# Optimization experiments

Hardware: AMD Instinct MI355X
Metric: run time of the kernel (lower is better)

The kernel has to match this reference:

```python
import jax, jax.numpy as jnp
import numpy as np

N, E, B, L = 65536, 262144, 512, 1000
IN_DIM, HID, VOCAB = 74, 128, 25
CHANNELS = [HID, 96, 128, IN_DIM, HID]  # protein conv1d filter chain


def _conv1d(x, k):
    # x: [B, C_in, L], k: [C_out, C_in, 3], stride 1, padding 1 (like nn.Conv1d)
    return jax.lax.conv_general_dilated(x, k, (1,), ((1, 1),),
                                        dimension_numbers=('NCH', 'OIH', 'NCH'))


def setup_inputs() -> dict:
    key = jax.random.key(0)
    ks = jax.random.split(key, 20)

    def gl(k, shape, fan_in):
        return jax.random.normal(k, shape, jnp.float32) / np.float32(np.sqrt(fan_in))

    inp = {}
    inp['node_feats'] = jax.random.normal(ks[0], (N, IN_DIM), jnp.float32)
    # GraphConv (conv1): weight [in, hid]
    inp['W_gc'] = gl(ks[1], (IN_DIM, HID), IN_DIM)
    inp['b_gc'] = jnp.zeros((HID,), jnp.float32)
    # MLPNodeReadout: two linears (no activation between, per dgllife default)
    inp['W_ro_in'] = gl(ks[2], (HID, HID), HID)
    inp['b_ro_in'] = jnp.zeros((HID,), jnp.float32)
    inp['W_ro_out'] = gl(ks[3], (HID, HID), HID)
    inp['b_ro_out'] = jnp.zeros((HID,), jnp.float32)
    inp['Wc1'] = gl(ks[4], (HID, HID), HID); inp['bc1'] = jnp.zeros((HID,), jnp.float32)
    inp['Wc2'] = gl(ks[5], (HID, HID), HID); inp['bc2'] = jnp.zeros((HID,), jnp.float32)
    # protein embedding + 4 conv1d layers
    inp['embed'] = jax.random.normal(ks[6], (VOCAB, HID), jnp.float32)
    for i in range(4):
        cin, cout = CHANNELS[i], CHANNELS[i + 1]
        inp['K%d' % (i + 1)] = gl(ks[7 + i], (cout, cin, 3), cin * 3)
        inp['cb%d' % (i + 1)] = jnp.zeros((cout,), jnp.float32)
    # CPI head: Linear(2h,2h)+ReLU, Linear(2h,1)+Sigmoid
    inp['Wf1'] = gl(ks[11], (2 * HID, 2 * HID), 2 * HID); inp['bf1'] = jnp.zeros((2 * HID,), jnp.float32)
    inp['Wf2'] = gl(ks[12], (2 * HID, 1), 2 * HID); inp['bf2'] = jnp.zeros((1,), jnp.float32)
    # graph structure / protein tokens
    inp['edge_src'] = jax.random.randint(ks[13], (E,), 0, N, jnp.int32)
    inp['edge_dst'] = jax.random.randint(ks[14], (E,), 0, N, jnp.int32)
    inp['graph_ids'] = jnp.sort(jax.random.randint(ks[15], (N,), 0, B, jnp.int32))
    inp['protein_seq'] = jax.random.randint(ks[16], (B, L), 0, VOCAB, jnp.int32)
    return inp


def reference(node_feats, W_gc, b_gc, W_ro_in, b_ro_in, W_ro_out, b_ro_out,
              Wc1, bc1, Wc2, bc2, embed, K1, cb1, K2, cb2, K3, cb3, K4, cb4,
              Wf1, bf1, Wf2, bf2, edge_src, edge_dst, graph_ids, protein_seq):
    n = node_feats.shape[0]
    nb = protein_seq.shape[0]
    # dgl.add_self_loop: append self edges
    loop = jnp.arange(n, dtype=edge_src.dtype)
    src = jnp.concatenate([edge_src, loop])
    dst = jnp.concatenate([edge_dst, loop])
    ones = jnp.ones(src.shape[0], jnp.float32)
    deg_out = jax.ops.segment_sum(ones, src, n)  # out-degree (src norm)
    deg_in = jax.ops.segment_sum(ones, dst, n)   # in-degree (dst norm)
    h = node_feats * jax.lax.rsqrt(deg_out)[:, None]
    h = jax.ops.segment_sum(h[src], dst, n) * jax.lax.rsqrt(deg_in)[:, None]
    h = jax.nn.relu(h @ W_gc + b_gc)
    # MLPNodeReadout (sum over nodes per graph), then outer ReLU
    x = (h @ W_ro_in + b_ro_in) @ W_ro_out + b_ro_out
    hg = jax.nn.relu(jax.ops.segment_sum(x, graph_ids, nb))  # [B, HID]
    # compound FC layers (dropout = identity)
    cv = jax.nn.relu(hg @ Wc1 + bc1)
    cv = jax.nn.relu(cv @ Wc2 + bc2)
    pv = jnp.transpose(embed[protein_seq], (0, 2, 1))
    for K, b in ((K1, cb1), (K2, cb2), (K3, cb3), (K4, cb4)):
        pv = jax.nn.relu(_conv1d(pv, K) + b[None, :, None])
    pmax = jnp.max(pv, axis=-1)  # adaptive_max_pool1d(output_size=1) + squeeze
    # CPI head
    z = jnp.concatenate([cv, pmax], axis=1)  # [B, 2*HID]
    z = jax.nn.relu(z @ Wf1 + bf1)
    return jax.nn.sigmoid(z @ Wf2 + bf2)  # [B, 1]
```

## Files before the change

### kernel.cpp

```cpp
#include <hip/hip_runtime.h>
#include <math.h>

#define IN_DIM 74
#define HID 128
#define LSEQ 1000
#define RSA 272
#define RSB 208
#define TILE 50
#define R0 58
#define R1 56
#define R2 54
#define R3 52
#define NCHUNK 42
#define NGRP 14
#define WBUF_SZ 24576
#define LDS_BIAS 49152
#define LDS_ACT  50944
#define ACTA_SZ  15776
#define ACTB_SZ  11648
#define ACTB_BASE (LDS_ACT + 4*ACTA_SZ)
#define LDS_TOTAL (ACTB_BASE + 4*ACTB_SZ)

typedef unsigned int u32;
typedef unsigned short u16;

typedef __attribute__((ext_vector_type(8))) short bf16x8;
typedef __attribute__((ext_vector_type(4))) float f32x4;

__device__ __forceinline__ u16 f2bf(float f){
  u32 u = __float_as_uint(f);
  u32 r = (u + 0x7fffu + ((u >> 16) & 1u)) >> 16;
  return (u16)r;
}
__device__ __forceinline__ u32 pack2(float x, float y){
  return (u32)f2bf(x) | ((u32)f2bf(y) << 16);
}

__global__ void k_cnt_edge(const int* __restrict__ src, const int* __restrict__ dst,
                           int* out_cnt, int* in_cnt, int E){
  int e = blockIdx.x*256 + threadIdx.x;
  if (e < E){ atomicAdd(&out_cnt[src[e]], 1); atomicAdd(&in_cnt[dst[e]], 1); }
}
__global__ void k_nfs(const float* __restrict__ nf, const int* __restrict__ out_cnt,
                      float* __restrict__ nfs, int total){
  int idx = blockIdx.x*256 + threadIdx.x;
  if (idx < total){
    int i = idx / IN_DIM;
    nfs[idx] = nf[idx] * rsqrtf((float)out_cnt[i] + 1.f);
  }
}
__global__ void k_scan1(const int* __restrict__ cnt, int* pref, int* bsum, int N){
  __shared__ int buf[256];
  int t = threadIdx.x, i = blockIdx.x*256 + t;
  int v = (i < N) ? cnt[i] : 0;
  buf[t] = v; __syncthreads();
  for (int o = 1; o < 256; o <<= 1){
    int tv = (t >= o) ? buf[t-o] : 0;
    __syncthreads(); buf[t] += tv; __syncthreads();
  }
  if (i < N) pref[i] = buf[t] - v;
  if (t == 255) bsum[blockIdx.x] = buf[255];
}
__global__ void k_scan2(int* bsum, int nb){
  __shared__ int buf[1024];
  int t = threadIdx.x;
  int v = (t < nb) ? bsum[t] : 0;
  buf[t] = v; __syncthreads();
  for (int o = 1; o < 1024; o <<= 1){
    int tv = (t >= o) ? buf[t-o] : 0;
    __syncthreads(); buf[t] += tv; __syncthreads();
  }
  if (t < nb) bsum[t] = buf[t] - v;
}
__global__ void k_scan3(const int* __restrict__ pref, const int* __restrict__ bsum,
                        int* offs, int* cur, int N){
  int i = blockIdx.x*256 + threadIdx.x;
  if (i < N){ int o = pref[i] + bsum[blockIdx.x]; offs[i] = o; cur[i] = o; }
}
__global__ void k_csr_fill(const int* __restrict__ src, const int* __restrict__ dst,
                           int* cur, int* csr_src, int E){
  int e = blockIdx.x*256 + threadIdx.x;
  if (e < E){ int slot = atomicAdd(&cur[dst[e]], 1); csr_src[slot] = src[e]; }
}

__global__ __launch_bounds__(256) void k_mega(const float* __restrict__ nfs,
    const int* __restrict__ csr_src, const int* __restrict__ offs,
    const int* __restrict__ in_cnt,
    const float* __restrict__ W, const float* __restrict__ bias,
    const int* __restrict__ gid, float* __restrict__ S, int N){
  __shared__ float Wl[IN_DIM*HID];
  __shared__ float rowsT[IN_DIM][36];
  __shared__ int lgid[32];
  const int tid = threadIdx.x;
  const int base = blockIdx.x * 32;
  for (int i = tid; i < IN_DIM*HID; i += 256) Wl[i] = W[i];
  if (tid < 32) lgid[tid] = (base + tid < N) ? gid[base + tid] : 0;

  int wid = tid >> 6, lane = tid & 63;
  for (int nn = wid; nn < 32; nn += 4){
    int d = base + nn;
    float a0 = 0.f, a1 = 0.f;
    if (d < N){
      int beg = offs[d], num = in_cnt[d];
      const float* row = nfs + (size_t)d*IN_DIM;
      a0 = row[lane];
      if (lane < IN_DIM-64) a1 = row[64+lane];
      for (int j = 0; j < num; ++j){
        int s = csr_src[beg + j];
        const float* rs = nfs + (size_t)s*IN_DIM;
        a0 += rs[lane];
        if (lane < IN_DIM-64) a1 += rs[64+lane];
      }
      float sc = rsqrtf((float)num + 1.f);
      a0 *= sc; a1 *= sc;
    }
    rowsT[lane][nn] = a0;
    if (lane < IN_DIM-64) rowsT[64+lane][nn] = a1;
  }
  __syncthreads();

  int c = tid & 127, rh = tid >> 7;
  float acc[16];
  #pragma unroll
  for (int i = 0; i < 16; ++i) acc[i] = 0.f;
  for (int k = 0; k < IN_DIM; ++k){
    float w = Wl[k*HID + c];
    const float4* rp = (const float4*)&rowsT[k][rh*16];
    float4 r0 = rp[0], r1 = rp[1], r2 = rp[2], r3 = rp[3];
    acc[0] += r0.x*w; acc[1] += r0.y*w; acc[2] += r0.z*w; acc[3] += r0.w*w;
    acc[4] += r1.x*w; acc[5] += r1.y*w; acc[6] += r1.z*w; acc[7] += r1.w*w;
    acc[8] += r2.x*w; acc[9] += r2.y*w; acc[10] += r2.z*w; acc[11] += r2.w*w;
    acc[12] += r3.x*w; acc[13] += r3.y*w; acc[14] += r3.z*w; acc[15] += r3.w*w;
  }
  float bv = bias[c];
  float run = 0.f;
  int curg = lgid[rh*16];
  #pragma unroll
  for (int i = 0; i < 16; ++i){
    int node = rh*16 + i;
    if (base + node >= N) break;
    int g = lgid[node];
    if (g != curg){
      if (run != 0.f) atomicAdd(&S[(size_t)curg*HID + c], run);
      run = 0.f; curg = g;
    }
    run += fmaxf(acc[i] + bv, 0.f);
  }
  if (run != 0.f) atomicAdd(&S[(size_t)curg*HID + c], run);
}

__global__ __launch_bounds__(128) void k_graph_tail(const float* __restrict__ S,
    const int* __restrict__ gid,
    const float* __restrict__ W_ri, const float* __restrict__ b_ri,
    const float* __restrict__ W_ro, const float* __restrict__ b_ro,
    const float* __restrict__ Wc1, const float* __restrict__ bc1,
    const float* __restrict__ Wc2, const float* __restrict__ bc2,
    float* __restrict__ z, int N){
  __shared__ float va[128], vb[128];
  __shared__ int bounds[2];
  int g = blockIdx.x, c = threadIdx.x;
  if (c < 2){
    int target = g + c, lo = 0, hi = N;
    while (lo < hi){ int mid = (lo+hi)>>1; if (gid[mid] < target) lo = mid+1; else hi = mid; }
    bounds[c] = lo;
  }
  __syncthreads();
  float cn = (float)(bounds[1] - bounds[0]);
  va[c] = S[(size_t)g*HID + c];
  __syncthreads();
  float s = 0.f;
  for (int k = 0; k < 128; ++k) s += va[k]*W_ri[k*128 + c];
  vb[c] = s + b_ri[c]*cn;
  __syncthreads();
  s = 0.f;
  for (int k = 0; k < 128; ++k) s += vb[k]*W_ro[k*128 + c];
  va[c] = fmaxf(s + b_ro[c]*cn, 0.f);
  __syncthreads();
  s = 0.f;
  for (int k = 0; k < 128; ++k) s += va[k]*Wc1[k*128 + c];
  vb[c] = fmaxf(s + bc1[c], 0.f);
  __syncthreads();
  s = 0.f;
  for (int k = 0; k < 128; ++k) s += vb[k]*Wc2[k*128 + c];
  z[(size_t)g*256 + c] = fmaxf(s + bc2[c], 0.f);
}

__global__ void k_setup(const float* __restrict__ K1, const float* __restrict__ K2,
                        const float* __restrict__ K3, const float* __restrict__ K4,
                        const float* __restrict__ cb1, const float* __restrict__ cb2,
                        const float* __restrict__ cb3, const float* __restrict__ cb4,
                        u16* __restrict__ AW, float* __restrict__ ball,
                        float* __restrict__ z, float* __restrict__ S,
                        int* __restrict__ out_cnt, int* __restrict__ in_cnt,
                        int N, int B){
  int idx = blockIdx.x*256 + threadIdx.x;
  if (idx < NCHUNK*4096){
    int g = idx >> 12, rem = idx & 4095;
    int co = rem >> 5, kk = rem & 31;
    const float* Kw; int CIN, CPAD, COUT, ksl;
    if (g < 12)      { Kw = K1; CIN = 128; CPAD = 128; COUT =  96; ksl = g; }
    else if (g < 21) { Kw = K2; CIN =  96; CPAD =  96; COUT = 128; ksl = g-12; }
    else if (g < 33) { Kw = K3; CIN =  74; CPAD = 128; COUT =  74; ksl = g-21; }
    else             { Kw = K4; CIN =  74; CPAD =  96; COUT = 128; ksl = g-33; }
    int k = ksl*32 + kk;
    int t = k / CPAD, ci = k - t*CPAD;
    float v = (co < COUT && ci < CIN) ? Kw[((size_t)co*CIN + ci)*3 + t] : 0.f;
    int sl2 = (kk >> 3) ^ ((co >> 1) & 3);
    AW[(size_t)g*4096 + co*32 + sl2*8 + (kk & 7)] = f2bf(v);
    return;
  }
  idx -= NCHUNK*4096;
  if (idx < 448){
    float v = 0.f;
    if (idx < 96) v = cb1[idx];
    else if (idx < 224) v = cb2[idx-96];
    else if (idx < 320){ int c = idx-224; v = (c < 74) ? cb3[c] : 0.f; }
    else v = cb4[idx-320];
    ball[idx] = v;
    return;
  }
  idx -= 448;
  if (idx < B*128){ z[(size_t)(idx>>7)*256 + 128 + (idx&127)] = 0.f; return; }
  idx -= B*128;
  if (idx < B*128){ S[idx] = 0.f; return; }
  idx -= B*128;
  if (idx < 2*N){
    if (idx < N) out_cnt[idx] = 0; else in_cnt[idx-N] = 0;
  }
}

__device__ __forceinline__ void stage24k(char* lds, int tid, const u16* src, int pbuf){
  const char* s = (const char*)src;
  char* d = lds + pbuf*WBUF_SZ;
  #pragma unroll
  for (int i = 0; i < 3; ++i)
    __builtin_amdgcn_global_load_lds(
      (const __attribute__((address_space(1))) unsigned*)(s + i*8192 + tid*16),
      (__attribute__((address_space(3))) unsigned*)(d + i*8192 + tid*16), 16, 0, 0);
}

template<int KS, int G0, int M, int TPC, int RS_IN, int RCAP>
__device__ __forceinline__ void conv_phases(char* lds, const char* actIn,
    const u16* __restrict__ AW, int co0, int lm, int cg, int scg, int tid,
    f32x4 (&acc)[M][4])
{
  #pragma unroll
  for (int m = 0; m < M; ++m)
    #pragma unroll
    for (int n = 0; n < 4; ++n) acc[m][n] = (f32x4){0.f,0.f,0.f,0.f};
  #pragma unroll
  for (int ks = 0; ks < KS; ++ks){
    const int g = G0 + ks;
    const char* wb = lds + ((g/3)&1)*WBUF_SZ + (g%3)*8192;
    bf16x8 Af[M];
    #pragma unroll
    for (int m = 0; m < M; ++m)
      Af[m] = *(const bf16x8*)(wb + (co0 + m*16 + lm)*64 + scg*16);
    const int tap = ks / TPC;
    const int c16 = (ks - tap*TPC)*4 + cg;
    bf16x8 Bf[4];
    #pragma unroll
    for (int n = 0; n < 4; ++n){
      int raw = n*16 + lm + tap;
      int row = raw < RCAP ? raw : RCAP;
      Bf[n] = *(const bf16x8*)(actIn + row*RS_IN + c16*16);
    }
    __builtin_amdgcn_s_setprio(1);
    #pragma unroll
    for (int m = 0; m < M; ++m)
      #pragma unroll
      for (int n = 0; n < 4; ++n)
        acc[m][n] = __builtin_amdgcn_mfma_f32_16x16x32_bf16(Af[m], Bf[n], acc[m][n], 0, 0, 0);
    __builtin_amdgcn_s_setprio(0);
    if ((g % 3) == 2 && (ks + 1 < KS)){
      __syncthreads();
      const int gn = g/3 + 2;
      if (gn < NGRP) stage24k(lds, tid, AW + (size_t)gn*12288, gn & 1);
    }
  }
}

template<int M>
__device__ __forceinline__ void epi_store(char* actOut, int RS_OUT,
    const float* lbias, int boff, int co0, int lm, int cg,
    int lbase, int nrows, f32x4 (&acc)[M][4])
{
  #pragma unroll
  for (int m = 0; m < M; ++m){
    int co = co0 + m*16 + cg*4;
    float4 bb = *(const float4*)(lbias + boff + co);
    #pragma unroll
    for (int n = 0; n < 4; ++n){
      int r1 = n*16 + lm;
      if (r1 < nrows){
        int l = lbase + r1;
        u32 lo = 0, hi = 0;
        if ((unsigned)l < (unsigned)LSEQ){
          f32x4 a = acc[m][n];
          lo = pack2(fmaxf(a[0]+bb.x, 0.f), fmaxf(a[1]+bb.y, 0.f));
          hi = pack2(fmaxf(a[2]+bb.z, 0.f), fmaxf(a[3]+bb.w, 0.f));
        }
        uint2 st; st.x = lo; st.y = hi;
        *(uint2*)(actOut + r1*RS_OUT + co*2) = st;
      }
    }
  }
}

__device__ __forceinline__ void epi_pool(const float* lbias, int boff,
    int co0, int lm, int cg, int l0, float* __restrict__ z, int b, f32x4 (&acc)[4][4])
{
  float mxv[4][4];
  #pragma unroll
  for (int m = 0; m < 4; ++m)
    #pragma unroll
    for (int j = 0; j < 4; ++j) mxv[m][j] = 0.f;
  #pragma unroll
  for (int m = 0; m < 4; ++m){
    float4 bb = *(const float4*)(lbias + boff + co0 + m*16 + cg*4);
    const float* bv = (const float*)&bb;
    #pragma unroll
    for (int n = 0; n < 4; ++n){
      int r1 = n*16 + lm;
      int l = l0 + r1;
      if (r1 < TILE && l < LSEQ){
        #pragma unroll
        for (int j = 0; j < 4; ++j)
          mxv[m][j] = fmaxf(mxv[m][j], fmaxf(acc[m][n][j] + bv[j], 0.f));
      }
    }
  }
  #pragma unroll
  for (int o = 1; o <= 8; o <<= 1)
    #pragma unroll
    for (int m = 0; m < 4; ++m)
      #pragma unroll
      for (int j = 0; j < 4; ++j)
        mxv[m][j] = fmaxf(mxv[m][j], __shfl_xor(mxv[m][j], o));
  if (lm == 0){
    float* zrow = z + (size_t)b*256 + 128;
    #pragma unroll
    for (int m = 0; m < 4; ++m)
      #pragma unroll
      for (int j = 0; j < 4; ++j)
        atomicMax((u32*)(zrow + co0 + m*16 + cg*4 + j), __float_as_uint(mxv[m][j]));
  }
}

__global__ __launch_bounds__(512, 1) void k_protein(
    const int* __restrict__ seq, const float* __restrict__ emb,
    const u16* __restrict__ AW, const float* __restrict__ ball,
    float* __restrict__ z)
{
  __shared__ __align__(16) char lds[LDS_TOTAL];
  const int tid = threadIdx.x;
  const int lane = tid & 63, wid = tid >> 6;
  const int lm = lane & 15, cg = lane >> 4;
  const int scg = cg ^ ((lm >> 1) & 3);
  const int tl = wid >> 1;
  const int h  = wid & 1;
  const int b  = blockIdx.y;
  const int l0 = (blockIdx.x*4 + tl) * TILE;

  for (int i = tid; i < 448; i += 512) ((float*)(lds + LDS_BIAS))[i] = ball[i];

  for (int idx = tid; idx < 4*R0*16; idx += 512){
    int t2 = idx / (R0*16), rem = idx - t2*(R0*16);
    int r = rem >> 4, p = rem & 15;
    int ll0 = (blockIdx.x*4 + t2) * TILE;
    int l = ll0 - 4 + r;
    uint4 st = make_uint4(0u,0u,0u,0u);
    if ((unsigned)l < (unsigned)LSEQ){
      int tok = seq[b*LSEQ + l];
      const float4* e = (const float4*)(emb + (size_t)tok*HID + p*8);
      float4 v0 = e[0], v1 = e[1];
      st.x = pack2(v0.x, v0.y); st.y = pack2(v0.z, v0.w);
      st.z = pack2(v1.x, v1.y); st.w = pack2(v1.z, v1.w);
    }
    *(uint4*)(lds + LDS_ACT + t2*ACTA_SZ + r*RSA + p*16) = st;
  }
  stage24k(lds, tid, AW, 0);
  stage24k(lds, tid, AW + 12288, 1);
  __syncthreads();

  char* actA = lds + LDS_ACT + tl*ACTA_SZ;
  char* actB = lds + ACTB_BASE + tl*ACTB_SZ;
  const float* lbias = (const float*)(lds + LDS_BIAS);

  {
    f32x4 acc[3][4];
    conv_phases<12,0,3,4,RSA,R0-1>(lds, actA, AW, h*48, lm, cg, scg, tid, acc);
    epi_store<3>(actB, RSB, lbias, 0, h*48, lm, cg, l0-3, R1, acc);
    __syncthreads();
    stage24k(lds, tid, AW + (size_t)5*12288, 5 & 1);
  }
  {
    f32x4 acc[4][4];
    conv_phases<9,12,4,3,RSB,R1-1>(lds, actB, AW, h*64, lm, cg, scg, tid, acc);
    epi_store<4>(actA, RSA, lbias, 96, h*64, lm, cg, l0-2, R2, acc);
    __syncthreads();
    stage24k(lds, tid, AW + (size_t)8*12288, 8 & 1);
  }
  {
    f32x4 acc[3][4];
    conv_phases<12,21,3,4,RSA,R2-1>(lds, actA, AW, h*48, lm, cg, scg, tid, acc);
    epi_store<3>(actB, RSB, lbias, 224, h*48, lm, cg, l0-1, R3, acc);
    __syncthreads();
    stage24k(lds, tid, AW + (size_t)12*12288, 12 & 1);
  }
  {
    f32x4 acc[4][4];
    conv_phases<9,33,4,3,RSB,R3-1>(lds, actB, AW, h*64, lm, cg, scg, tid, acc);
    epi_pool(lbias, 320, h*64, lm, cg, l0, z, b, acc);
  }
}

__global__ __launch_bounds__(256) void k_fc_head(const float* __restrict__ z,
    const float* __restrict__ Wf1, const float* __restrict__ bf1,
    const float* __restrict__ Wf2, const float* __restrict__ bf2v,
    float* __restrict__ out){
  __shared__ float za[256];
  __shared__ float red[4];
  int r = blockIdx.x, c = threadIdx.x;
  za[c] = z[(size_t)r*256 + c];
  __syncthreads();
  float s = 0.f;
  for (int k = 0; k < 256; ++k) s += za[k]*Wf1[(size_t)k*256 + c];
  s = fmaxf(s + bf1[c], 0.f);
  float p = s * Wf2[c];
  for (int o = 32; o; o >>= 1) p += __shfl_xor(p, o);
  if ((c & 63) == 0) red[c >> 6] = p;
  __syncthreads();
  if (c == 0) out[r] = 1.f/(1.f + __expf(-(red[0]+red[1]+red[2]+red[3] + bf2v[0])));
}

extern "C" void kernel_launch(void* const* d_in, const int* in_sizes, int n_in,
                              void* d_out, int out_size, void* d_ws, size_t ws_size,
                              hipStream_t stream){
  const float* nf   = (const float*)d_in[0];
  const float* W_gc = (const float*)d_in[1];
  const float* b_gc = (const float*)d_in[2];
  const float* W_ri = (const float*)d_in[3];
  const float* b_ri = (const float*)d_in[4];
  const float* W_ro = (const float*)d_in[5];
  const float* b_ro = (const float*)d_in[6];
  const float* Wc1  = (const float*)d_in[7];
  const float* bc1  = (const float*)d_in[8];
  const float* Wc2  = (const float*)d_in[9];
  const float* bc2  = (const float*)d_in[10];
  const float* emb  = (const float*)d_in[11];
  const float* K1 = (const float*)d_in[12]; const float* cb1 = (const float*)d_in[13];
  const float* K2 = (const float*)d_in[14]; const float* cb2 = (const float*)d_in[15];
  const float* K3 = (const float*)d_in[16]; const float* cb3 = (const float*)d_in[17];
  const float* K4 = (const float*)d_in[18]; const float* cb4 = (const float*)d_in[19];
  const float* Wf1 = (const float*)d_in[20]; const float* bf1 = (const float*)d_in[21];
  const float* Wf2 = (const float*)d_in[22]; const float* bf2v = (const float*)d_in[23];
  const int* esrc = (const int*)d_in[24];
  const int* edst = (const int*)d_in[25];
  const int* gids = (const int*)d_in[26];
  const int* seq  = (const int*)d_in[27];
  float* out = (float*)d_out;

  int N = in_sizes[26];
  int E = in_sizes[24];
  int B = out_size;
  int nb = (N + 255)/256;

  char* ws = (char*)d_ws;
  size_t off = 0;
  auto take = [&](size_t bytes)->char*{
    char* p = ws + off; off = (off + bytes + 255) & ~(size_t)255; return p;
  };
  float* z      = (float*)take((size_t)B*2*HID*4);
  float* S      = (float*)take((size_t)B*HID*4);
  int* out_cnt  = (int*)take((size_t)N*4);
  int* in_cnt   = (int*)take((size_t)N*4);
  int* pref     = (int*)take((size_t)N*4);
  int* offs     = (int*)take((size_t)N*4);
  int* cur      = (int*)take((size_t)N*4);
  int* bsum     = (int*)take(1024*4);
  int* csr_src  = (int*)take((size_t)E*4);
  u16* AW       = (u16*)take((size_t)NCHUNK*8192);
  float* ball   = (float*)take(448*4);
  float* nfs    = (float*)take((size_t)N*IN_DIM*4);

  int setup_total = NCHUNK*4096 + 448 + B*128 + B*128 + 2*N;
  k_setup<<<(setup_total+255)/256, 256, 0, stream>>>(K1, K2, K3, K4, cb1, cb2, cb3, cb4,
                                                     AW, ball, z, S, out_cnt, in_cnt, N, B);

  k_cnt_edge<<<(E+255)/256, 256, 0, stream>>>(esrc, edst, out_cnt, in_cnt, E);
  k_nfs<<<((N*IN_DIM)+255)/256, 256, 0, stream>>>(nf, out_cnt, nfs, N*IN_DIM);
  k_scan1<<<nb, 256, 0, stream>>>(in_cnt, pref, bsum, N);
  k_scan2<<<1, 1024, 0, stream>>>(bsum, nb);
  k_scan3<<<nb, 256, 0, stream>>>(pref, bsum, offs, cur, N);
  k_csr_fill<<<(E+255)/256, 256, 0, stream>>>(esrc, edst, cur, csr_src, E);
  k_mega<<<(N+31)/32, 256, 0, stream>>>(nfs, csr_src, offs, in_cnt,
                                        W_gc, b_gc, gids, S, N);
  k_graph_tail<<<B, 128, 0, stream>>>(S, gids, W_ri, b_ri, W_ro, b_ro,
                                      Wc1, bc1, Wc2, bc2, z, N);

  dim3 pgrid(5, B);
  k_protein<<<pgrid, 512, 0, stream>>>(seq, emb, AW, ball, z);

  k_fc_head<<<B, 256, 0, stream>>>(z, Wf1, bf1, Wf2, bf2v, out);
}
```

Before: 408.0 us.

## Fuse graph-branch kernels into one cooperative persistent kernel with grid syncs

Replaces the ten separate graph-branch launches (setup, degree count, normalization, three-stage scan, CSR fill, aggregation+GEMM, graph tail) with a single cooperative kernel of 512 blocks that uses grid-wide barriers between phases. This removes per-launch overhead and inter-kernel gaps. In exchange every phase runs on a fixed 512-block grid with grid-stride loops, which may reduce parallelism for the larger phases. The big shared-memory footprint may also limit co-residency, and the block-level scan assumes nb fits in 256.

Result: slower. 804.5 us (+97.2%).

```diff
diff --git a/kernel.cpp b/kernel.cpp
--- a/kernel.cpp
+++ b/kernel.cpp
@@ -1,5 +1,8 @@
 #include <hip/hip_runtime.h>
+#include <hip/hip_cooperative_groups.h>
 #include <math.h>
+
+namespace cg = cooperative_groups;
 
 #define IN_DIM 74
 #define HID 128
@@ -36,196 +39,207 @@
   return (u32)f2bf(x) | ((u32)f2bf(y) << 16);
 }
 
-__global__ void k_cnt_edge(const int* __restrict__ src, const int* __restrict__ dst,
-                           int* out_cnt, int* in_cnt, int E){
-  int e = blockIdx.x*256 + threadIdx.x;
-  if (e < E){ atomicAdd(&out_cnt[src[e]], 1); atomicAdd(&in_cnt[dst[e]], 1); }
-}
-__global__ void k_nfs(const float* __restrict__ nf, const int* __restrict__ out_cnt,
-                      float* __restrict__ nfs, int total){
-  int idx = blockIdx.x*256 + threadIdx.x;
-  if (idx < total){
-    int i = idx / IN_DIM;
-    nfs[idx] = nf[idx] * rsqrtf((float)out_cnt[i] + 1.f);
-  }
-}
-__global__ void k_scan1(const int* __restrict__ cnt, int* pref, int* bsum, int N){
-  __shared__ int buf[256];
-  int t = threadIdx.x, i = blockIdx.x*256 + t;
-  int v = (i < N) ? cnt[i] : 0;
-  buf[t] = v; __syncthreads();
-  for (int o = 1; o < 256; o <<= 1){
-    int tv = (t >= o) ? buf[t-o] : 0;
-    __syncthreads(); buf[t] += tv; __syncthreads();
-  }
-  if (i < N) pref[i] = buf[t] - v;
-  if (t == 255) bsum[blockIdx.x] = buf[255];
-}
-__global__ void k_scan2(int* bsum, int nb){
-  __shared__ int buf[1024];
-  int t = threadIdx.x;
-  int v = (t < nb) ? bsum[t] : 0;
-  buf[t] = v; __syncthreads();
-  for (int o = 1; o < 1024; o <<= 1){
-    int tv = (t >= o) ? buf[t-o] : 0;
-    __syncthreads(); buf[t] += tv; __syncthreads();
-  }
-  if (t < nb) bsum[t] = buf[t] - v;
-}
-__global__ void k_scan3(const int* __restrict__ pref, const int* __restrict__ bsum,
-                        int* offs, int* cur, int N){
-  int i = blockIdx.x*256 + threadIdx.x;
-  if (i < N){ int o = pref[i] + bsum[blockIdx.x]; offs[i] = o; cur[i] = o; }
-}
-__global__ void k_csr_fill(const int* __restrict__ src, const int* __restrict__ dst,
-                           int* cur, int* csr_src, int E){
-  int e = blockIdx.x*256 + threadIdx.x;
-  if (e < E){ int slot = atomicAdd(&cur[dst[e]], 1); csr_src[slot] = src[e]; }
-}
-
-__global__ __launch_bounds__(256) void k_mega(const float* __restrict__ nfs,
-    const int* __restrict__ csr_src, const int* __restrict__ offs,
-    const int* __restrict__ in_cnt,
-    const float* __restrict__ W, const float* __restrict__ bias,
-    const int* __restrict__ gid, float* __restrict__ S, int N){
-  __shared__ float Wl[IN_DIM*HID];
-  __shared__ float rowsT[IN_DIM][36];
-  __shared__ int lgid[32];
-  const int tid = threadIdx.x;
-  const int base = blockIdx.x * 32;
-  for (int i = tid; i < IN_DIM*HID; i += 256) Wl[i] = W[i];
-  if (tid < 32) lgid[tid] = (base + tid < N) ? gid[base + tid] : 0;
-
-  int wid = tid >> 6, lane = tid & 63;
-  for (int nn = wid; nn < 32; nn += 4){
-    int d = base + nn;
-    float a0 = 0.f, a1 = 0.f;
-    if (d < N){
-      int beg = offs[d], num = in_cnt[d];
-      const float* row = nfs + (size_t)d*IN_DIM;
-      a0 = row[lane];
-      if (lane < IN_DIM-64) a1 = row[64+lane];
-      for (int j = 0; j < num; ++j){
-        int s = csr_src[beg + j];
-        const float* rs = nfs + (size_t)s*IN_DIM;
-        a0 += rs[lane];
-        if (lane < IN_DIM-64) a1 += rs[64+lane];
-      }
-      float sc = rsqrtf((float)num + 1.f);
-      a0 *= sc; a1 *= sc;
-    }
-    rowsT[lane][nn] = a0;
-    if (lane < IN_DIM-64) rowsT[64+lane][nn] = a1;
-  }
-  __syncthreads();
-
-  int c = tid & 127, rh = tid >> 7;
-  float acc[16];
-  #pragma unroll
-  for (int i = 0; i < 16; ++i) acc[i] = 0.f;
-  for (int k = 0; k < IN_DIM; ++k){
-    float w = Wl[k*HID + c];
-    const float4* rp = (const float4*)&rowsT[k][rh*16];
-    float4 r0 = rp[0], r1 = rp[1], r2 = rp[2], r3 = rp[3];
-    acc[0] += r0.x*w; acc[1] += r0.y*w; acc[2] += r0.z*w; acc[3] += r0.w*w;
-    acc[4] += r1.x*w; acc[5] += r1.y*w; acc[6] += r1.z*w; acc[7] += r1.w*w;
-    acc[8] += r2.x*w; acc[9] += r2.y*w; acc[10] += r2.z*w; acc[11] += r2.w*w;
-    acc[12] += r3.x*w; acc[13] += r3.y*w; acc[14] += r3.z*w; acc[15] += r3.w*w;
-  }
-  float bv = bias[c];
-  float run = 0.f;
-  int curg = lgid[rh*16];
-  #pragma unroll
-  for (int i = 0; i < 16; ++i){
-    int node = rh*16 + i;
-    if (base + node >= N) break;
-    int g = lgid[node];
-    if (g != curg){
-      if (run != 0.f) atomicAdd(&S[(size_t)curg*HID + c], run);
-      run = 0.f; curg = g;
-    }
-    run += fmaxf(acc[i] + bv, 0.f);
-  }
-  if (run != 0.f) atomicAdd(&S[(size_t)curg*HID + c], run);
-}
-
-__global__ __launch_bounds__(128) void k_graph_tail(const float* __restrict__ S,
+__global__ __launch_bounds__(256) void k_graph_all(
+    const float* __restrict__ K1, const float* __restrict__ K2,
+    const float* __restrict__ K3, const float* __restrict__ K4,
+    const float* __restrict__ cb1, const float* __restrict__ cb2,
+    const float* __restrict__ cb3, const float* __restrict__ cb4,
+    u16* __restrict__ AW, float* __restrict__ ball,
+    float* __restrict__ z, float* __restrict__ S,
+    int* __restrict__ out_cnt, int* __restrict__ in_cnt,
+    const float* __restrict__ nf, float* __restrict__ nfs,
+    const int* __restrict__ esrc, const int* __restrict__ edst,
+    int* __restrict__ pref, int* __restrict__ bsum,
+    int* __restrict__ offs, int* __restrict__ cur, int* __restrict__ csr_src,
+    const float* __restrict__ W_gc, const float* __restrict__ b_gc,
     const int* __restrict__ gid,
     const float* __restrict__ W_ri, const float* __restrict__ b_ri,
     const float* __restrict__ W_ro, const float* __restrict__ b_ro,
     const float* __restrict__ Wc1, const float* __restrict__ bc1,
     const float* __restrict__ Wc2, const float* __restrict__ bc2,
-    float* __restrict__ z, int N){
-  __shared__ float va[128], vb[128];
-  __shared__ int bounds[2];
-  int g = blockIdx.x, c = threadIdx.x;
-  if (c < 2){
-    int target = g + c, lo = 0, hi = N;
-    while (lo < hi){ int mid = (lo+hi)>>1; if (gid[mid] < target) lo = mid+1; else hi = mid; }
-    bounds[c] = lo;
-  }
-  __syncthreads();
-  float cn = (float)(bounds[1] - bounds[0]);
-  va[c] = S[(size_t)g*HID + c];
-  __syncthreads();
-  float s = 0.f;
-  for (int k = 0; k < 128; ++k) s += va[k]*W_ri[k*128 + c];
-  vb[c] = s + b_ri[c]*cn;
-  __syncthreads();
-  s = 0.f;
-  for (int k = 0; k < 128; ++k) s += vb[k]*W_ro[k*128 + c];
-  va[c] = fmaxf(s + b_ro[c]*cn, 0.f);
-  __syncthreads();
-  s = 0.f;
-  for (int k = 0; k < 128; ++k) s += va[k]*Wc1[k*128 + c];
-  vb[c] = fmaxf(s + bc1[c], 0.f);
-  __syncthreads();
-  s = 0.f;
-  for (int k = 0; k < 128; ++k) s += vb[k]*Wc2[k*128 + c];
-  z[(size_t)g*256 + c] = fmaxf(s + bc2[c], 0.f);
-}
-
-__global__ void k_setup(const float* __restrict__ K1, const float* __restrict__ K2,
-                        const float* __restrict__ K3, const float* __restrict__ K4,
-                        const float* __restrict__ cb1, const float* __restrict__ cb2,
-                        const float* __restrict__ cb3, const float* __restrict__ cb4,
-                        u16* __restrict__ AW, float* __restrict__ ball,
-                        float* __restrict__ z, float* __restrict__ S,
-                        int* __restrict__ out_cnt, int* __restrict__ in_cnt,
-                        int N, int B){
-  int idx = blockIdx.x*256 + threadIdx.x;
-  if (idx < NCHUNK*4096){
-    int g = idx >> 12, rem = idx & 4095;
-    int co = rem >> 5, kk = rem & 31;
-    const float* Kw; int CIN, CPAD, COUT, ksl;
-    if (g < 12)      { Kw = K1; CIN = 128; CPAD = 128; COUT =  96; ksl = g; }
-    else if (g < 21) { Kw = K2; CIN =  96; CPAD =  96; COUT = 128; ksl = g-12; }
-    else if (g < 33) { Kw = K3; CIN =  74; CPAD = 128; COUT =  74; ksl = g-21; }
-    else             { Kw = K4; CIN =  74; CPAD =  96; COUT = 128; ksl = g-33; }
-    int k = ksl*32 + kk;
-    int t = k / CPAD, ci = k - t*CPAD;
-    float v = (co < COUT && ci < CIN) ? Kw[((size_t)co*CIN + ci)*3 + t] : 0.f;
-    int sl2 = (kk >> 3) ^ ((co >> 1) & 3);
-    AW[(size_t)g*4096 + co*32 + sl2*8 + (kk & 7)] = f2bf(v);
-    return;
-  }
-  idx -= NCHUNK*4096;
-  if (idx < 448){
-    float v = 0.f;
-    if (idx < 96) v = cb1[idx];
-    else if (idx < 224) v = cb2[idx-96];
-    else if (idx < 320){ int c = idx-224; v = (c < 74) ? cb3[c] : 0.f; }
-    else v = cb4[idx-320];
-    ball[idx] = v;
-    return;
-  }
-  idx -= 448;
-  if (idx < B*128){ z[(size_t)(idx>>7)*256 + 128 + (idx&127)] = 0.f; return; }
-  idx -= B*128;
-  if (idx < B*128){ S[idx] = 0.f; return; }
-  idx -= B*128;
-  if (idx < 2*N){
-    if (idx < N) out_cnt[idx] = 0; else in_cnt[idx-N] = 0;
+    int N, int E, int B, int nb)
+{
+  cg::grid_group gg = cg::this_grid();
+  __shared__ float Wl[IN_DIM*HID];
+  __shared__ float rowsT[IN_DIM][36];
+  __shared__ int lgid[32];
+  __shared__ int sbuf[256];
+  __shared__ float tva[128], tvb[128];
+  __shared__ int tbounds[2];
+  const int tid = threadIdx.x;
+  const int gsz = gridDim.x * 256;
+  const int g0  = blockIdx.x * 256 + tid;
+
+  for (int i = tid; i < IN_DIM*HID; i += 256) Wl[i] = W_gc[i];
+
+  const int setup_total = NCHUNK*4096 + 448 + B*128 + B*128 + 2*N;
+  for (int idx = g0; idx < setup_total; idx += gsz){
+    int t = idx;
+    if (t < NCHUNK*4096){
+      int g = t >> 12, rem = t & 4095;
+      int co = rem >> 5, kk = rem & 31;
+      const float* Kw; int CIN, CPAD, COUT, ksl;
+      if (g < 12)      { Kw = K1; CIN = 128; CPAD = 128; COUT =  96; ksl = g; }
+      else if (g < 21) { Kw = K2; CIN =  96; CPAD =  96; COUT = 128; ksl = g-12; }
+      else if (g < 33) { Kw = K3; CIN =  74; CPAD = 128; COUT =  74; ksl = g-21; }
+      else             { Kw = K4; CIN =  74; CPAD =  96; COUT = 128; ksl = g-33; }
+      int k = ksl*32 + kk;
+      int tp = k / CPAD, ci = k - tp*CPAD;
+      float v = (co < COUT && ci < CIN) ? Kw[((size_t)co*CIN + ci)*3 + tp] : 0.f;
+      int sl2 = (kk >> 3) ^ ((co >> 1) & 3);
+      AW[(size_t)g*4096 + co*32 + sl2*8 + (kk & 7)] = f2bf(v);
+      continue;
+    }
+    t -= NCHUNK*4096;
+    if (t < 448){
+      float v = 0.f;
+      if (t < 96) v = cb1[t];
+      else if (t < 224) v = cb2[t-96];
+      else if (t < 320){ int c = t-224; v = (c < 74) ? cb3[c] : 0.f; }
+      else v = cb4[t-320];
+      ball[t] = v;
+      continue;
+    }
+    t -= 448;
+    if (t < B*128){ z[(size_t)(t>>7)*256 + 128 + (t&127)] = 0.f; continue; }
+    t -= B*128;
+    if (t < B*128){ S[t] = 0.f; continue; }
+    t -= B*128;
+    if (t < N) out_cnt[t] = 0; else in_cnt[t-N] = 0;
+  }
+  gg.sync();
+
+  for (int e = g0; e < E; e += gsz){
+    atomicAdd(&out_cnt[esrc[e]], 1);
+    atomicAdd(&in_cnt[edst[e]], 1);
+  }
+  gg.sync();
+
+  for (int v = blockIdx.x; v < nb; v += gridDim.x){
+    int i = v*256 + tid;
+    int val = (i < N) ? in_cnt[i] : 0;
+    sbuf[tid] = val; __syncthreads();
+    for (int o = 1; o < 256; o <<= 1){
+      int tv = (tid >= o) ? sbuf[tid-o] : 0;
+      __syncthreads(); sbuf[tid] += tv; __syncthreads();
+    }
+    if (i < N) pref[i] = sbuf[tid] - val;
+    if (tid == 255) bsum[v] = sbuf[255];
+    __syncthreads();
+  }
+  for (int idx = g0; idx < N*IN_DIM; idx += gsz)
+    nfs[idx] = nf[idx] * rsqrtf((float)out_cnt[idx / IN_DIM] + 1.f);
+  gg.sync();
+
+  if (blockIdx.x == 0){
+    int val = (tid < nb) ? bsum[tid] : 0;
+    sbuf[tid] = val; __syncthreads();
+    for (int o = 1; o < 256; o <<= 1){
+      int tv = (tid >= o) ? sbuf[tid-o] : 0;
+      __syncthreads(); sbuf[tid] += tv; __syncthreads();
+    }
+    if (tid < nb) bsum[tid] = sbuf[tid] - val;
+  }
+  gg.sync();
+
+  for (int i = g0; i < N; i += gsz){
+    int o = pref[i] + bsum[i >> 8];
+    offs[i] = o; cur[i] = o;
+  }
+  gg.sync();
+
+  for (int e = g0; e < E; e += gsz){
+    int slot = atomicAdd(&cur[edst[e]], 1);
+    csr_src[slot] = esrc[e];
+  }
+  gg.sync();
+
+  const int NB32 = (N + 31) >> 5;
+  for (int v = blockIdx.x; v < NB32; v += gridDim.x){
+    const int base = v * 32;
+    if (tid < 32) lgid[tid] = (base + tid < N) ? gid[base + tid] : 0;
+    int wid = tid >> 6, lane = tid & 63;
+    for (int nn = wid; nn < 32; nn += 4){
+      int d = base + nn;
+      float a0 = 0.f, a1 = 0.f;
+      if (d < N){
+        int beg = offs[d], num = in_cnt[d];
+        const float* row = nfs + (size_t)d*IN_DIM;
+        a0 = row[lane];
+        if (lane < IN_DIM-64) a1 = row[64+lane];
+        for (int j = 0; j < num; ++j){
+          int s = csr_src[beg + j];
+          const float* rs = nfs + (size_t)s*IN_DIM;
+          a0 += rs[lane];
+          if (lane < IN_DIM-64) a1 += rs[64+lane];
+        }
+        float sc = rsqrtf((float)num + 1.f);
+        a0 *= sc; a1 *= sc;
+      }
+      rowsT[lane][nn] = a0;
+      if (lane < IN_DIM-64) rowsT[64+lane][nn] = a1;
+    }
+    __syncthreads();
+
+    int c = tid & 127, rh = tid >> 7;
+    float acc[16];
+    #pragma unroll
+    for (int i = 0; i < 16; ++i) acc[i] = 0.f;
+    for (int k = 0; k < IN_DIM; ++k){
+      float w = Wl[k*HID + c];
+      const float4* rp = (const float4*)&rowsT[k][rh*16];
+      float4 r0 = rp[0], r1 = rp[1], r2 = rp[2], r3 = rp[3];
+      acc[0] += r0.x*w; acc[1] += r0.y*w; acc[2] += r0.z*w; acc[3] += r0.w*w;
+      acc[4] += r1.x*w; acc[5] += r1.y*w; acc[6] += r1.z*w; acc[7] += r1.w*w;
+      acc[8] += r2.x*w; acc[9] += r2.y*w; acc[10] += r2.z*w; acc[11] += r2.w*w;
+      acc[12] += r3.x*w; acc[13] += r3.y*w; acc[14] += r3.z*w; acc[15] += r3.w*w;
+    }
+    float bv = b_gc[c];
+    float run = 0.f;
+    int curg = lgid[rh*16];
+    #pragma unroll
+    for (int i = 0; i < 16; ++i){
+      int node = rh*16 + i;
+      if (base + node >= N) break;
+      int gq = lgid[node];
+      if (gq != curg){
+        if (run != 0.f) atomicAdd(&S[(size_t)curg*HID + c], run);
+        run = 0.f; curg = gq;
+      }
+      run += fmaxf(acc[i] + bv, 0.f);
+    }
+    if (run != 0.f) atomicAdd(&S[(size_t)curg*HID + c], run);
+    __syncthreads();
+  }
+  gg.sync();
+
+  for (int g = blockIdx.x; g < B; g += gridDim.x){
+    int c = tid & 127;
+    if (tid < 2){
+      int target = g + tid, lo = 0, hi = N;
+      while (lo < hi){ int mid = (lo+hi)>>1; if (gid[mid] < target) lo = mid+1; else hi = mid; }
+      tbounds[tid] = lo;
+    }
+    __syncthreads();
+    float cn = (float)(tbounds[1] - tbounds[0]);
+    if (tid < 128) tva[c] = S[(size_t)g*HID + c];
+    __syncthreads();
+    float s = 0.f;
+    for (int k = 0; k < 128; ++k) s += tva[k]*W_ri[k*128 + c];
+    if (tid < 128) tvb[c] = s + b_ri[c]*cn;
+    __syncthreads();
+    s = 0.f;
+    for (int k = 0; k < 128; ++k) s += tvb[k]*W_ro[k*128 + c];
+    if (tid < 128) tva[c] = fmaxf(s + b_ro[c]*cn, 0.f);
+    __syncthreads();
+    s = 0.f;
+    for (int k = 0; k < 128; ++k) s += tva[k]*Wc1[k*128 + c];
+    if (tid < 128) tvb[c] = fmaxf(s + bc1[c], 0.f);
+    __syncthreads();
+    s = 0.f;
+    for (int k = 0; k < 128; ++k) s += tvb[k]*Wc2[k*128 + c];
+    if (tid < 128) z[(size_t)g*256 + c] = fmaxf(s + bc2[c], 0.f);
+    __syncthreads();
   }
 }
 
@@ -484,20 +498,21 @@
   float* ball   = (float*)take(448*4);
   float* nfs    = (float*)take((size_t)N*IN_DIM*4);
 
-  int setup_total = NCHUNK*4096 + 448 + B*128 + B*128 + 2*N;
-  k_setup<<<(setup_total+255)/256, 256, 0, stream>>>(K1, K2, K3, K4, cb1, cb2, cb3, cb4,
-                                                     AW, ball, z, S, out_cnt, in_cnt, N, B);
-
-  k_cnt_edge<<<(E+255)/256, 256, 0, stream>>>(esrc, edst, out_cnt, in_cnt, E);
-  k_nfs<<<((N*IN_DIM)+255)/256, 256, 0, stream>>>(nf, out_cnt, nfs, N*IN_DIM);
-  k_scan1<<<nb, 256, 0, stream>>>(in_cnt, pref, bsum, N);
-  k_scan2<<<1, 1024, 0, stream>>>(bsum, nb);
-  k_scan3<<<nb, 256, 0, stream>>>(pref, bsum, offs, cur, N);
-  k_csr_fill<<<(E+255)/256, 256, 0, stream>>>(esrc, edst, cur, csr_src, E);
-  k_mega<<<(N+31)/32, 256, 0, stream>>>(nfs, csr_src, offs, in_cnt,
-                                        W_gc, b_gc, gids, S, N);
-  k_graph_tail<<<B, 128, 0, stream>>>(S, gids, W_ri, b_ri, W_ro, b_ro,
-                                      Wc1, bc1, Wc2, bc2, z, N);
+  void* kargs[] = {
+    (void*)&K1, (void*)&K2, (void*)&K3, (void*)&K4,
+    (void*)&cb1, (void*)&cb2, (void*)&cb3, (void*)&cb4,
+    (void*)&AW, (void*)&ball, (void*)&z, (void*)&S,
+    (void*)&out_cnt, (void*)&in_cnt,
+    (void*)&nf, (void*)&nfs,
+    (void*)&esrc, (void*)&edst,
+    (void*)&pref, (void*)&bsum, (void*)&offs, (void*)&cur, (void*)&csr_src,
+    (void*)&W_gc, (void*)&b_gc, (void*)&gids,
+    (void*)&W_ri, (void*)&b_ri, (void*)&W_ro, (void*)&b_ro,
+    (void*)&Wc1, (void*)&bc1, (void*)&Wc2, (void*)&bc2,
+    (void*)&N, (void*)&E, (void*)&B, (void*)&nb
+  };
+  hipLaunchCooperativeKernel((void*)k_graph_all, dim3(512), dim3(256),
+                             kargs, 0, stream);
 
   dim3 pgrid(5, B);
   k_protein<<<pgrid, 512, 0, stream>>>(seq, emb, AW, ball, z);
```
